# Kernel tuning notes

Measured on AMD Instinct MI355X. Metric: run time of the kernel, lower is better.

The kernel has to match this reference:

```python
import jax, jax.numpy as jnp
import numpy as np

B, L, D_MODEL, N_HEADS = 2, 1024, 1024, 8
KH = D_MODEL // 2 // N_HEADS   # key head dim = 64
VH = D_MODEL // N_HEADS        # value head dim = 128
SCALING = KH ** -0.5


def setup_inputs() -> dict:
    key = jax.random.key(0)
    ks = jax.random.split(key, 9)
    def w(k, shp):
        return jax.random.normal(k, shp, dtype=jnp.float32) / np.float32(np.sqrt(shp[0]))
    return {
        "x": jax.random.normal(ks[0], (B, L, D_MODEL), dtype=jnp.float32),
        "Wq": w(ks[1], (D_MODEL, D_MODEL // 2)),
        "Wk": w(ks[2], (D_MODEL, D_MODEL // 2)),
        "Wg1": w(ks[3], (D_MODEL, 16)),
        "Wg2": w(ks[4], (16, D_MODEL // 2)),
        "Wv": w(ks[5], (D_MODEL, D_MODEL)),
        "Wgp": w(ks[6], (D_MODEL, D_MODEL)),
        "bgp": jnp.zeros((D_MODEL,), jnp.float32),
        "Wout": w(ks[7], (D_MODEL, D_MODEL)),
    }


def _split_heads(t):
    # (b, l, h*d) -> (b, h, l, d)
    b, l, _ = t.shape
    return t.reshape(b, l, N_HEADS, -1).transpose(0, 2, 1, 3)


def _forward(x, Wq, Wk, Wg1, Wg2, Wv, Wgp, bgp, Wout):
    q = _split_heads(x @ Wq)                    # b h l kd
    k = _split_heads(x @ Wk) * SCALING          # b h l kd
    kg = _split_heads((x @ Wg1) @ Wg2)          # b h l kd (low-rank gate)
    v = _split_heads(x @ Wv)                    # b h l vd
    g = jax.nn.silu(x @ Wgp + bgp)              # b l d
    # per-head scalar decay gate in (0,1)
    gate = jnp.exp(jnp.mean(jax.nn.log_sigmoid(kg), axis=-1, keepdims=True) / 16.0)  # b h l 1
    prefix = jnp.cumprod(gate + 1e-6, axis=2)[..., None]                              # b h l 1 1
    kv = jnp.einsum('bhld,bhle->bhlde', k, v)                                         # b h l kd vd
    state = jnp.cumsum(kv / prefix, axis=2) * prefix                                  # decayed running KV state
    out = jnp.einsum('bhld,bhlde->bhle', q, state)                                    # b h l vd
    # LayerNorm over value head dim, no affine, eps=1e-5
    mu = out.mean(-1, keepdims=True)
    var = out.var(-1, keepdims=True)
    out = (out - mu) * jax.lax.rsqrt(var + 1e-5)
    out = out.transpose(0, 2, 1, 3).reshape(x.shape[0], x.shape[1], D_MODEL)
    return (g * out) @ Wout


def reference(x, Wq, Wk, Wg1, Wg2, Wv, Wgp, bgp, Wout):
    return _forward(x, Wq, Wk, Wg1, Wg2, Wv, Wgp, bgp, Wout)
```

## Files before the change

kernel.cpp:

```cpp
#include <hip/hip_runtime.h>

typedef __bf16 bf16x8 __attribute__((ext_vector_type(8)));
typedef float floatx4 __attribute__((ext_vector_type(4)));

__device__ __forceinline__ ushort f2bf(float f) {
  union { float f; unsigned u; } a; a.f = f;
  unsigned u = a.u;
  unsigned r = (u + 0x7FFFu + ((u >> 16) & 1u)) >> 16;
  return (ushort)r;
}
__device__ __forceinline__ float bf2f(ushort u) {
  union { unsigned u; float f; } a; a.u = ((unsigned)u) << 16;
  return a.f;
}

__device__ __forceinline__ void gl_lds16(const ushort* g, ushort* l) {
  __builtin_amdgcn_global_load_lds((const __attribute__((address_space(1))) void*)g,
                                   (__attribute__((address_space(3))) void*)l, 16, 0, 0);
}

#define SWZH(row, col, stride) ((((row) * (stride)) + (col)) ^ (((row) & 7) << 3))
#define SWZC(row, col) ((((row) * 128) + (col)) ^ ((((row) >> 3) & 7) << 2))


__global__ __launch_bounds__(256) void prep_all_kernel(
    const float* __restrict__ x,
    const float* __restrict__ Wq, const float* __restrict__ Wk,
    const float* __restrict__ Wv, const float* __restrict__ Wgp,
    const float* __restrict__ Wout,
    const float* __restrict__ Wg1, const float* __restrict__ Wg2,
    ushort* __restrict__ WcatT, ushort* __restrict__ WoutT,
    float* __restrict__ gamma, ushort* __restrict__ xb) {
  __shared__ __align__(16) float smem[1344];
  int bid = blockIdx.x;
  int tid = threadIdx.x;

  if (bid < 4096) {
    int nv = (bid & 127) * 32, k0 = (bid >> 7) * 32;
    const float* W; ushort* dst; int N, ncol, nrow; float scale = 1.f;
    if (nv < 512)       { W = Wq;   N = 512;  ncol = nv;         nrow = nv;        dst = WcatT; }
    else if (nv < 1024) { W = Wk;   N = 512;  ncol = nv - 512;   nrow = nv;        dst = WcatT; scale = 0.125f; }
    else if (nv < 2048) { W = Wv;   N = 1024; ncol = nv - 1024;  nrow = nv;        dst = WcatT; }
    else if (nv < 3072) { W = Wgp;  N = 1024; ncol = nv - 2048;  nrow = nv;        dst = WcatT; }
    else                { W = Wout; N = 1024; ncol = nv - 3072;  nrow = nv - 3072; dst = WoutT; }
    float* tile = smem;
    int xi = tid & 31, yi = tid >> 5;
    #pragma unroll
    for (int i = 0; i < 32; i += 8)
      tile[(yi + i) * 33 + xi] = W[(size_t)(k0 + yi + i) * N + ncol + xi];
    __syncthreads();
    #pragma unroll
    for (int i = 0; i < 32; i += 8)
      dst[(size_t)(nrow + yi + i) * 1024 + k0 + xi] = f2bf(tile[xi * 33 + yi + i] * scale);
    return;
  }

  int rowi = bid - 4096;
  int b = rowi >> 10, l = rowi & 1023;
  float* xrow = smem;
  float* part = smem + 1024;
  float* tsh  = smem + 1296;

  {
    float4 v = *(const float4*)(x + (size_t)rowi * 1024 + tid * 4);
    ushort4 o;
    o.x = f2bf(v.x); o.y = f2bf(v.y); o.z = f2bf(v.z); o.w = f2bf(v.w);
    *(ushort4*)(xb + (size_t)rowi * 1024 + tid * 4) = o;
    *(float4*)&xrow[tid * 4] = v;
  }
  __syncthreads();

  {
    int j = tid & 15, slice = tid >> 4;
    const float* xr = xrow + slice * 64;
    float p = 0.f;
    #pragma unroll 4
    for (int kk = 0; kk < 64; kk++)
      p += xr[kk] * Wg1[(size_t)(slice * 64 + kk) * 16 + j];
    part[slice * 17 + j] = p;
  }
  __syncthreads();
  if (tid < 16) {
    float s = 0.f;
    #pragma unroll
    for (int i = 0; i < 16; i++) s += part[i * 17 + tid];
    tsh[tid] = s;
  }
  __syncthreads();

  float ls0, ls1;
  {
    int n = tid;
    float kg = 0.f;
    #pragma unroll
    for (int j = 0; j < 16; j++) kg += tsh[j] * Wg2[j * 512 + n];
    ls0 = (kg >= 0.f) ? -log1pf(expf(-kg)) : (kg - log1pf(expf(kg)));
  }
  {
    int n = tid + 256;
    float kg = 0.f;
    #pragma unroll
    for (int j = 0; j < 16; j++) kg += tsh[j] * Wg2[j * 512 + n];
    ls1 = (kg >= 0.f) ? -log1pf(expf(-kg)) : (kg - log1pf(expf(kg)));
  }
  #pragma unroll
  for (int m = 32; m >= 1; m >>= 1) {
    ls0 += __shfl_xor(ls0, m);
    ls1 += __shfl_xor(ls1, m);
  }
  if ((tid & 63) == 0) {
    int w = tid >> 6;
    gamma[(size_t)(b * 8 + w) * 1024 + l]       = expf(ls0 * (1.f / 1024.f)) + 1e-6f;
    gamma[(size_t)(b * 8 + w + 4) * 1024 + l]   = expf(ls1 * (1.f / 1024.f)) + 1e-6f;
  }
}

__global__ __launch_bounds__(64) void prefix_kernel(const float* __restrict__ gamma,
                                                    float* __restrict__ af,
                                                    float* __restrict__ Atot) {
  int blk = blockIdx.x;
  int bh = blk >> 4, c = blk & 15;
  int lane = threadIdx.x;
  float g = gamma[(size_t)bh * 1024 + c * 64 + lane];
  #pragma unroll
  for (int m = 1; m < 64; m <<= 1) {
    float o = __shfl_up(g, m);
    if (lane >= m) g *= o;
  }
  af[(size_t)bh * 1024 + c * 64 + lane] = g;
  if (lane == 63) Atot[blk] = g;
}

__global__ __launch_bounds__(256) void gemm_proj_kernel(
    const ushort* __restrict__ A, const ushort* __restrict__ BT,
    const float* __restrict__ af, const float* __restrict__ Atot,
    const float* __restrict__ bgp,
    ushort* __restrict__ Qb, ushort* __restrict__ Kb,
    ushort* __restrict__ Ktb, ushort* __restrict__ Vtb,
    ushort* __restrict__ gsilu) {
  const int K = 1024;
  __shared__ __align__(16) char ldsraw[32768];
  ushort* As = (ushort*)ldsraw;
  ushort* Bs = (ushort*)(ldsraw + 8192);
  float*  Cs = (float*)ldsraw;
  __shared__ float ssh[2][64];
  __shared__ float bsh[128];

  int tid = threadIdx.x;
  int lane = tid & 63, wid = tid >> 6;
  int wr = wid >> 1, wc = wid & 1;
  int m0 = blockIdx.x * 64, n0 = blockIdx.y * 128;
  int by = blockIdx.y;
  int rtype = (by < 4) ? 0 : (by < 8) ? 1 : (by < 16) ? 2 : 3;
  int b = m0 >> 10, lbase = m0 & 1023, cch = lbase >> 6;

  if (rtype <= 1) {
    if (tid < 128) {
      int j = tid >> 6, li = tid & 63;
      int h = ((n0 - (rtype << 9)) >> 6) + j;
      int bh = b * 8 + h;
      float a = af[(size_t)bh * 1024 + lbase + li];
      ssh[j][li] = (rtype == 0) ? a : (Atot[bh * 16 + cch] / a);
    }
  } else if (rtype == 3) {
    if (tid < 128) bsh[tid] = bgp[n0 - 2048 + tid];
  }

  floatx4 acc[2][4];
  #pragma unroll
  for (int r = 0; r < 2; r++)
    #pragma unroll
    for (int c = 0; c < 4; c++)
      acc[r][c] = (floatx4){0.f, 0.f, 0.f, 0.f};

  int srA = wid * 16 + (lane >> 3);
  int srB = wid * 32 + (lane >> 3);
  int sc = (lane & 7) * 8;
  const ushort* ag = A + (size_t)(m0 + srA) * K + sc;
  const ushort* bg = BT + (size_t)(n0 + srB) * K + sc;
  ushort* asb = As + (wid * 16) * 64;
  ushort* bsb = Bs + (wid * 32) * 64;
  int row = lane & 15, kseg = (lane >> 4) << 3;

  for (int k0 = 0; k0 < K; k0 += 64) {
    __syncthreads();
    #pragma unroll
    for (int i = 0; i < 2; i++)
      gl_lds16(ag + (size_t)(i * 8) * K + k0, asb + i * 8 * 64);
    #pragma unroll
    for (int i = 0; i < 4; i++)
      gl_lds16(bg + (size_t)(i * 8) * K + k0, bsb + i * 8 * 64);
    __syncthreads();
    #pragma unroll
    for (int kk = 0; kk < 64; kk += 32) {
      bf16x8 av[2], bv[4];
      #pragma unroll
      for (int r = 0; r < 2; r++)
        av[r] = *(const bf16x8*)&As[(wr * 32 + r * 16 + row) * 64 + kk + kseg];
      #pragma unroll
      for (int c = 0; c < 4; c++)
        bv[c] = *(const bf16x8*)&Bs[(wc * 64 + c * 16 + row) * 64 + kk + kseg];
      #pragma unroll
      for (int r = 0; r < 2; r++)
        #pragma unroll
        for (int c = 0; c < 4; c++)
          acc[r][c] = __builtin_amdgcn_mfma_f32_16x16x32_bf16(av[r], bv[c], acc[r][c], 0, 0, 0);
    }
  }

  __syncthreads();
  #pragma unroll
  for (int r = 0; r < 2; r++) {
    int crow = wr * 32 + r * 16 + ((lane >> 4) << 2);
    #pragma unroll
    for (int c = 0; c < 4; c++) {
      int ccol = wc * 64 + c * 16 + (lane & 15);
      #pragma unroll
      for (int i = 0; i < 4; i++)
        Cs[SWZC(crow + i, ccol)] = acc[r][c][i];
    }
  }
  __syncthreads();

  if (rtype == 0) {
    #pragma unroll
    for (int it = 0; it < 4; it++) {
      int u = tid + it * 256;
      int rw = u >> 4, col8 = (u & 15) * 8;
      int hh = col8 >> 6, d = col8 & 63;
      float a = ssh[hh][rw];
      float4 v0 = *(const float4*)&Cs[SWZC(rw, col8)];
      float4 v1 = *(const float4*)&Cs[SWZC(rw, col8 + 4)];
      ushort o[8];
      o[0]=f2bf(v0.x*a); o[1]=f2bf(v0.y*a); o[2]=f2bf(v0.z*a); o[3]=f2bf(v0.w*a);
      o[4]=f2bf(v1.x*a); o[5]=f2bf(v1.y*a); o[6]=f2bf(v1.z*a); o[7]=f2bf(v1.w*a);
      int bh = b * 8 + (n0 >> 6) + hh;
      *(uint4*)(Qb + ((size_t)bh * 1024 + lbase + rw) * 64 + d) = *(uint4*)&o[0];
    }
  } else if (rtype == 1) {
    #pragma unroll
    for (int it = 0; it < 4; it++) {
      int u = tid + it * 256;
      int rw = u >> 4, col8 = (u & 15) * 8;
      int hh = col8 >> 6, d = col8 & 63;
      float4 v0 = *(const float4*)&Cs[SWZC(rw, col8)];
      float4 v1 = *(const float4*)&Cs[SWZC(rw, col8 + 4)];
      ushort o[8];
      o[0]=f2bf(v0.x); o[1]=f2bf(v0.y); o[2]=f2bf(v0.z); o[3]=f2bf(v0.w);
      o[4]=f2bf(v1.x); o[5]=f2bf(v1.y); o[6]=f2bf(v1.z); o[7]=f2bf(v1.w);
      int bh = b * 8 + ((n0 - 512) >> 6) + hh;
      *(uint4*)(Kb + ((size_t)bh * 1024 + lbase + rw) * 64 + d) = *(uint4*)&o[0];
    }
    #pragma unroll
    for (int it = 0; it < 4; it++) {
      int u = tid + it * 256;
      int l0 = (u & 7) * 8, dd = (u >> 3) & 63, hh = u >> 9;
      ushort o[8];
      #pragma unroll
      for (int j = 0; j < 8; j++)
        o[j] = f2bf(Cs[SWZC(l0 + j, hh * 64 + dd)] * ssh[hh][l0 + j]);
      int bh = b * 8 + ((n0 - 512) >> 6) + hh;
      *(uint4*)(Ktb + ((size_t)(bh * 64 + dd)) * 1024 + lbase + l0) = *(uint4*)&o[0];
    }
  } else if (rtype == 2) {
    #pragma unroll
    for (int it = 0; it < 4; it++) {
      int u = tid + it * 256;
      int l0 = (u & 7) * 8, e = u >> 3;
      ushort o[8];
      #pragma unroll
      for (int j = 0; j < 8; j++)
        o[j] = f2bf(Cs[SWZC(l0 + j, e)]);
      int bh = b * 8 + ((n0 - 1024) >> 7);
      *(uint4*)(Vtb + ((size_t)(bh * 128 + e)) * 1024 + lbase + l0) = *(uint4*)&o[0];
    }
  } else {
    #pragma unroll
    for (int it = 0; it < 4; it++) {
      int u = tid + it * 256;
      int rw = u >> 4, col8 = (u & 15) * 8;
      float4 v0 = *(const float4*)&Cs[SWZC(rw, col8)];
      float4 v1 = *(const float4*)&Cs[SWZC(rw, col8 + 4)];
      float vv[8] = {v0.x, v0.y, v0.z, v0.w, v1.x, v1.y, v1.z, v1.w};
      ushort o[8];
      #pragma unroll
      for (int j = 0; j < 8; j++) {
        float z = vv[j] + bsh[col8 + j];
        o[j] = f2bf(z / (1.f + expf(-z)));
      }
      *(uint4*)(gsilu + (size_t)(m0 + rw) * 1024 + (n0 - 2048) + col8) = *(uint4*)&o[0];
    }
  }
}

__global__ __launch_bounds__(256) void chunk_T_kernel(const ushort* __restrict__ Ktb,
                                                      const ushort* __restrict__ Vtb,
                                                      float* __restrict__ Tt) {
  int c = blockIdx.x, bh = blockIdx.y;
  int tid = threadIdx.x;
  int lane = tid & 63, wid = tid >> 6;
  int col_l = lane & 15, kseg8 = (lane >> 4) * 8;
  int d0w = wid * 16;

  __shared__ __align__(16) ushort Kt[64 * 64];
  __shared__ __align__(16) ushort Vs[128 * 64];

  #pragma unroll
  for (int i = 0; i < 2; i++) {
    int u = tid + i * 256;
    int row = u >> 3, col8 = u & 7;
    *(uint4*)&Kt[SWZH(row, col8 * 8, 64)] =
        *(const uint4*)(Ktb + ((size_t)(bh * 64 + row)) * 1024 + c * 64 + col8 * 8);
  }
  #pragma unroll
  for (int i = 0; i < 4; i++) {
    int u = tid + i * 256;
    int row = u >> 3, col8 = u & 7;
    *(uint4*)&Vs[SWZH(row, col8 * 8, 64)] =
        *(const uint4*)(Vtb + ((size_t)(bh * 128 + row)) * 1024 + c * 64 + col8 * 8);
  }
  __syncthreads();

  floatx4 acc[8];
  #pragma unroll
  for (int i = 0; i < 8; i++) acc[i] = (floatx4){0.f, 0.f, 0.f, 0.f};

  #pragma unroll
  for (int kk = 0; kk < 64; kk += 32) {
    bf16x8 kb = *(const bf16x8*)&Kt[SWZH(d0w + col_l, kk + kseg8, 64)];
    #pragma unroll
    for (int fe = 0; fe < 8; fe++) {
      bf16x8 vb = *(const bf16x8*)&Vs[SWZH(fe * 16 + col_l, kk + kseg8, 64)];
      acc[fe] = __builtin_amdgcn_mfma_f32_16x16x32_bf16(vb, kb, acc[fe], 0, 0, 0);
    }
  }

  float* To = Tt + (size_t)(bh * 16 + c) * 8192;
  #pragma unroll
  for (int fe = 0; fe < 8; fe++) {
    #pragma unroll
    for (int r = 0; r < 4; r++) {
      int e = fe * 16 + (lane >> 4) * 4 + r;
      To[(size_t)e * 64 + d0w + col_l] = acc[fe][r];
    }
  }
}

__global__ __launch_bounds__(256) void state_kernel(const float* __restrict__ Tt,
                                                    const float* __restrict__ Atot,
                                                    ushort* __restrict__ Stb) {
  int es = blockIdx.x, bh = blockIdx.y;
  int tid = threadIdx.x;
  size_t off = (size_t)es * 512 + tid * 2;
  float2 S = {0.f, 0.f};
  for (int c = 0; c < 16; c++) {
    float A = Atot[bh * 16 + c];
    size_t base = (size_t)(bh * 16 + c) * 8192 + off;
    ushort2 o; o.x = f2bf(S.x); o.y = f2bf(S.y);
    *(ushort2*)(Stb + base) = o;
    float2 t = *(const float2*)(Tt + base);
    S.x = A * S.x + t.x;
    S.y = A * S.y + t.y;
  }
}

__global__ __launch_bounds__(256) void out_chunk_kernel(const float* __restrict__ af,
                                                        const ushort* __restrict__ Qb,
                                                        const ushort* __restrict__ Kb,
                                                        const ushort* __restrict__ Stb,
                                                        const ushort* __restrict__ Vtb,
                                                        const ushort* __restrict__ gsilu,
                                                        ushort* __restrict__ gout) {
  int c = blockIdx.x, bh = blockIdx.y;
  int b = bh >> 3, h = bh & 7;
  int tid = threadIdx.x;
  int lane = tid & 63, wid = tid >> 6;
  int col_l = lane & 15, kseg8 = (lane >> 4) * 8;
  int t0w = wid * 16;

  __shared__ __align__(16) ushort Qs[64 * 64];
  __shared__ __align__(16) ushort Ks[64 * 64];
  __shared__ __align__(16) ushort Ss[128 * 64];
  __shared__ __align__(16) ushort Vs[128 * 64];
  __shared__ __align__(16) ushort Ps[64 * 64];
  __shared__ __align__(16) ushort Gz[64 * 128];
  __shared__ float inva_sh[64];

  #pragma unroll
  for (int i = 0; i < 2; i++) {
    int u = tid + i * 256;
    int row = u >> 3, col8 = u & 7;
    *(uint4*)&Qs[SWZH(row, col8 * 8, 64)] =
        *(const uint4*)(Qb + ((size_t)(bh * 1024 + c * 64 + row)) * 64 + col8 * 8);
    *(uint4*)&Ks[SWZH(row, col8 * 8, 64)] =
        *(const uint4*)(Kb + ((size_t)(bh * 1024 + c * 64 + row)) * 64 + col8 * 8);
  }
  #pragma unroll
  for (int i = 0; i < 4; i++) {
    int u = tid + i * 256;
    int row = u >> 3, col8 = u & 7;
    *(uint4*)&Ss[SWZH(row, col8 * 8, 64)] =
        *(const uint4*)(Stb + (size_t)(bh * 16 + c) * 8192 + (size_t)row * 64 + col8 * 8);
    *(uint4*)&Vs[SWZH(row, col8 * 8, 64)] =
        *(const uint4*)(Vtb + ((size_t)(bh * 128 + row)) * 1024 + c * 64 + col8 * 8);
  }
  #pragma unroll
  for (int i = 0; i < 4; i++) {
    int u = tid + i * 256;
    int row = u >> 4, ch = u & 15;
    *(uint4*)&Gz[SWZH(row, ch * 8, 128)] =
        *(const uint4*)(gsilu + ((size_t)(b * 1024 + c * 64 + row)) * 1024 + h * 128 + ch * 8);
  }
  if (tid < 64) inva_sh[tid] = 1.f / af[(size_t)bh * 1024 + c * 64 + tid];
  __syncthreads();

  floatx4 pacc[4];
  floatx4 acc[8];
  #pragma unroll
  for (int i = 0; i < 4; i++) pacc[i] = (floatx4){0.f, 0.f, 0.f, 0.f};
  #pragma unroll
  for (int i = 0; i < 8; i++) acc[i] = (floatx4){0.f, 0.f, 0.f, 0.f};

  #pragma unroll
  for (int kk = 0; kk < 64; kk += 32) {
    bf16x8 qb = *(const bf16x8*)&Qs[SWZH(t0w + col_l, kk + kseg8, 64)];
    #pragma unroll
    for (int fs = 0; fs < 4; fs++) {
      bf16x8 kb = *(const bf16x8*)&Ks[SWZH(fs * 16 + col_l, kk + kseg8, 64)];
      pacc[fs] = __builtin_amdgcn_mfma_f32_16x16x32_bf16(kb, qb, pacc[fs], 0, 0, 0);
    }
    #pragma unroll
    for (int fe = 0; fe < 8; fe++) {
      bf16x8 sb = *(const bf16x8*)&Ss[SWZH(fe * 16 + col_l, kk + kseg8, 64)];
      acc[fe] = __builtin_amdgcn_mfma_f32_16x16x32_bf16(sb, qb, acc[fe], 0, 0, 0);
    }
  }

  int tl = t0w + col_l;
  #pragma unroll
  for (int fs = 0; fs < 4; fs++) {
    ushort o[4];
    #pragma unroll
    for (int r = 0; r < 4; r++) {
      int s = fs * 16 + (lane >> 4) * 4 + r;
      float pv = (s <= tl) ? pacc[fs][r] * inva_sh[s] : 0.f;
      o[r] = f2bf(pv);
    }
    int s0 = fs * 16 + (lane >> 4) * 4;
    *(ushort4*)&Ps[SWZH(tl, s0, 64)] = *(ushort4*)&o[0];
  }
  __syncthreads();

  #pragma unroll
  for (int kk = 0; kk < 64; kk += 32) {
    bf16x8 pb = *(const bf16x8*)&Ps[SWZH(t0w + col_l, kk + kseg8, 64)];
    #pragma unroll
    for (int fe = 0; fe < 8; fe++) {
      bf16x8 vb = *(const bf16x8*)&Vs[SWZH(fe * 16 + col_l, kk + kseg8, 64)];
      acc[fe] = __builtin_amdgcn_mfma_f32_16x16x32_bf16(vb, pb, acc[fe], 0, 0, 0);
    }
  }
  __syncthreads();

  float s1 = 0.f, s2 = 0.f;
  #pragma unroll
  for (int fe = 0; fe < 8; fe++)
    #pragma unroll
    for (int r = 0; r < 4; r++) {
      float v = acc[fe][r];
      s1 += v; s2 += v * v;
    }
  s1 += __shfl_xor(s1, 16); s2 += __shfl_xor(s2, 16);
  s1 += __shfl_xor(s1, 32); s2 += __shfl_xor(s2, 32);
  float mu = s1 * (1.f / 128.f);
  float var = s2 * (1.f / 128.f) - mu * mu;
  float rs = rsqrtf(var + 1e-5f);

  ushort* Gs = Vs;
  #pragma unroll
  for (int fe = 0; fe < 8; fe++)
    #pragma unroll
    for (int r = 0; r < 4; r++) {
      int e = fe * 16 + (lane >> 4) * 4 + r;
      float y = (acc[fe][r] - mu) * rs;
      float g = bf2f(Gz[SWZH(tl, e, 128)]);
      Gs[SWZH(tl, e, 128)] = f2bf(y * g);
    }
  __syncthreads();

  #pragma unroll
  for (int i = 0; i < 4; i++) {
    int u = tid + i * 256;
    int row = u >> 4, ch = u & 15;
    *(uint4*)(gout + ((size_t)(b * 1024 + c * 64 + row)) * 1024 + h * 128 + ch * 8) =
        *(uint4*)&Gs[SWZH(row, ch * 8, 128)];
  }
}

__global__ __launch_bounds__(256) void gemm_out_kernel(const ushort* __restrict__ A,
                                                       const ushort* __restrict__ BT,
                                                       float* __restrict__ C) {
  const int K = 1024, N = 1024;
  __shared__ __align__(16) ushort As[64 * 64];
  __shared__ __align__(16) ushort Bs[128 * 64];
  int tid = threadIdx.x;
  int lane = tid & 63, wid = tid >> 6;
  int wr = wid >> 1, wc = wid & 1;
  int m0 = blockIdx.x * 64, n0 = blockIdx.y * 128;
  int row = lane & 15, kseg = (lane >> 4) << 3;

  floatx4 acc[2][4];
  #pragma unroll
  for (int r = 0; r < 2; r++)
    #pragma unroll
    for (int c = 0; c < 4; c++)
      acc[r][c] = (floatx4){0.f, 0.f, 0.f, 0.f};

  int srowA = wid * 16 + (lane >> 3);
  int srowB = wid * 32 + (lane >> 3);
  int scol = (lane & 7) * 8;
  const ushort* ag = A + (size_t)(m0 + srowA) * K + scol;
  const ushort* bg = BT + (size_t)(n0 + srowB) * K + scol;
  ushort* asb = As + (wid * 16) * 64;
  ushort* bsb = Bs + (wid * 32) * 64;

  for (int k0 = 0; k0 < K; k0 += 64) {
    __syncthreads();
    #pragma unroll
    for (int i = 0; i < 2; i++)
      gl_lds16(ag + (size_t)(i * 8) * K + k0, asb + i * 8 * 64);
    #pragma unroll
    for (int i = 0; i < 4; i++)
      gl_lds16(bg + (size_t)(i * 8) * K + k0, bsb + i * 8 * 64);
    __syncthreads();
    #pragma unroll
    for (int kk = 0; kk < 64; kk += 32) {
      bf16x8 av[2], bv[4];
      #pragma unroll
      for (int r = 0; r < 2; r++)
        av[r] = *(const bf16x8*)&As[(wr * 32 + r * 16 + row) * 64 + kk + kseg];
      #pragma unroll
      for (int c = 0; c < 4; c++)
        bv[c] = *(const bf16x8*)&Bs[(wc * 64 + c * 16 + row) * 64 + kk + kseg];
      #pragma unroll
      for (int r = 0; r < 2; r++)
        #pragma unroll
        for (int c = 0; c < 4; c++)
          acc[r][c] = __builtin_amdgcn_mfma_f32_16x16x32_bf16(av[r], bv[c], acc[r][c], 0, 0, 0);
    }
  }

  int r4 = (lane >> 4) << 2;
  #pragma unroll
  for (int r = 0; r < 2; r++)
    #pragma unroll
    for (int c = 0; c < 4; c++) {
      int crow = m0 + wr * 32 + r * 16 + r4;
      int ccol = n0 + wc * 64 + c * 16 + (lane & 15);
      #pragma unroll
      for (int i = 0; i < 4; i++)
        C[(size_t)(crow + i) * N + ccol] = acc[r][c][i];
    }
}

extern "C" void kernel_launch(void* const* d_in, const int* in_sizes, int n_in,
                              void* d_out, int out_size, void* d_ws, size_t ws_size,
                              hipStream_t stream) {
  const float* x    = (const float*)d_in[0];
  const float* Wq   = (const float*)d_in[1];
  const float* Wk   = (const float*)d_in[2];
  const float* Wg1  = (const float*)d_in[3];
  const float* Wg2  = (const float*)d_in[4];
  const float* Wv   = (const float*)d_in[5];
  const float* Wgp  = (const float*)d_in[6];
  const float* bgp  = (const float*)d_in[7];
  const float* Wout = (const float*)d_in[8];
  float* out = (float*)d_out;

  char* ws = (char*)d_ws;
  float*  Tt     = (float*)(ws + 0);
  ushort* Stb    = (ushort*)(ws + 8388608);
  float*  gamma  = (float*)(ws + 12582912);
  float*  af     = (float*)(ws + 12648448);
  float*  Atot   = (float*)(ws + 12713984);
  ushort* Qb     = (ushort*)(ws + 12718080);
  ushort* Kb     = (ushort*)(ws + 14815232);
  ushort* Ktb    = (ushort*)(ws + 16912384);
  ushort* Vtb    = (ushort*)(ws + 19009536);
  ushort* xb     = (ushort*)(ws + 23203840);
  ushort* WcatT  = (ushort*)(ws + 27398144);
  ushort* WoutT  = (ushort*)(ws + 33689600);
  ushort* gout   = (ushort*)(ws + 35786752);
  ushort* gsilu  = (ushort*)(ws + 39981056);

  prep_all_kernel<<<6144, 256, 0, stream>>>(x, Wq, Wk, Wv, Wgp, Wout, Wg1, Wg2,
                                            WcatT, WoutT, gamma, xb);
  prefix_kernel<<<256, 64, 0, stream>>>(gamma, af, Atot);

  gemm_proj_kernel<<<dim3(32, 24), 256, 0, stream>>>(xb, WcatT, af, Atot, bgp,
                                                     Qb, Kb, Ktb, Vtb, gsilu);

  chunk_T_kernel<<<dim3(16, 16), 256, 0, stream>>>(Ktb, Vtb, Tt);
  state_kernel<<<dim3(16, 16), 256, 0, stream>>>(Tt, Atot, Stb);
  out_chunk_kernel<<<dim3(16, 16), 256, 0, stream>>>(af, Qb, Kb, Stb, Vtb, gsilu, gout);

  gemm_out_kernel<<<dim3(32, 8), 256, 0, stream>>>(gout, WoutT, out);
}
```

Baseline: 87.41 us.

## Fuse prefix scan into consumer kernels and double threads in chunk kernels

```diff
diff --git a/kernel.cpp b/kernel.cpp
--- a/kernel.cpp
+++ b/kernel.cpp
@@ -17,6 +17,16 @@
 __device__ __forceinline__ void gl_lds16(const ushort* g, ushort* l) {
   __builtin_amdgcn_global_load_lds((const __attribute__((address_space(1))) void*)g,
                                    (__attribute__((address_space(3))) void*)l, 16, 0, 0);
+}
+
+__device__ __forceinline__ float chunk_scan(float g) {
+  int lane = threadIdx.x & 63;
+  #pragma unroll
+  for (int m = 1; m < 64; m <<= 1) {
+    float o = __shfl_up(g, m);
+    if (lane >= m) g *= o;
+  }
+  return g;
 }
 
 #define SWZH(row, col, stride) ((((row) * (stride)) + (col)) ^ (((row) & 7) << 3))
@@ -115,26 +125,9 @@
   }
 }
 
-__global__ __launch_bounds__(64) void prefix_kernel(const float* __restrict__ gamma,
-                                                    float* __restrict__ af,
-                                                    float* __restrict__ Atot) {
-  int blk = blockIdx.x;
-  int bh = blk >> 4, c = blk & 15;
-  int lane = threadIdx.x;
-  float g = gamma[(size_t)bh * 1024 + c * 64 + lane];
-  #pragma unroll
-  for (int m = 1; m < 64; m <<= 1) {
-    float o = __shfl_up(g, m);
-    if (lane >= m) g *= o;
-  }
-  af[(size_t)bh * 1024 + c * 64 + lane] = g;
-  if (lane == 63) Atot[blk] = g;
-}
-
 __global__ __launch_bounds__(256) void gemm_proj_kernel(
     const ushort* __restrict__ A, const ushort* __restrict__ BT,
-    const float* __restrict__ af, const float* __restrict__ Atot,
-    const float* __restrict__ bgp,
+    const float* __restrict__ gamma, const float* __restrict__ bgp,
     ushort* __restrict__ Qb, ushort* __restrict__ Kb,
     ushort* __restrict__ Ktb, ushort* __restrict__ Vtb,
     ushort* __restrict__ gsilu) {
@@ -152,16 +145,14 @@
   int m0 = blockIdx.x * 64, n0 = blockIdx.y * 128;
   int by = blockIdx.y;
   int rtype = (by < 4) ? 0 : (by < 8) ? 1 : (by < 16) ? 2 : 3;
-  int b = m0 >> 10, lbase = m0 & 1023, cch = lbase >> 6;
-
-  if (rtype <= 1) {
-    if (tid < 128) {
-      int j = tid >> 6, li = tid & 63;
-      int h = ((n0 - (rtype << 9)) >> 6) + j;
-      int bh = b * 8 + h;
-      float a = af[(size_t)bh * 1024 + lbase + li];
-      ssh[j][li] = (rtype == 0) ? a : (Atot[bh * 16 + cch] / a);
-    }
+  int b = m0 >> 10, lbase = m0 & 1023;
+
+  if (rtype <= 1 && wid < 2) {
+    int h = ((n0 - (rtype << 9)) >> 6) + wid;
+    int bh = b * 8 + h;
+    float a = chunk_scan(gamma[(size_t)bh * 1024 + lbase + lane]);
+    float Ac = __shfl(a, 63);
+    ssh[wid][lane] = (rtype == 0) ? a : (Ac / a);
   } else if (rtype == 3) {
     if (tid < 128) bsh[tid] = bgp[n0 - 2048 + tid];
   }
@@ -293,68 +284,78 @@
   }
 }
 
-__global__ __launch_bounds__(256) void chunk_T_kernel(const ushort* __restrict__ Ktb,
+__global__ __launch_bounds__(512) void chunk_T_kernel(const ushort* __restrict__ Ktb,
                                                       const ushort* __restrict__ Vtb,
                                                       float* __restrict__ Tt) {
   int c = blockIdx.x, bh = blockIdx.y;
   int tid = threadIdx.x;
   int lane = tid & 63, wid = tid >> 6;
+  int wq = wid & 3, eh = wid >> 2;
   int col_l = lane & 15, kseg8 = (lane >> 4) * 8;
-  int d0w = wid * 16;
+  int d0w = wq * 16;
 
   __shared__ __align__(16) ushort Kt[64 * 64];
   __shared__ __align__(16) ushort Vs[128 * 64];
 
-  #pragma unroll
-  for (int i = 0; i < 2; i++) {
-    int u = tid + i * 256;
-    int row = u >> 3, col8 = u & 7;
+  {
+    int row = tid >> 3, col8 = tid & 7;
     *(uint4*)&Kt[SWZH(row, col8 * 8, 64)] =
         *(const uint4*)(Ktb + ((size_t)(bh * 64 + row)) * 1024 + c * 64 + col8 * 8);
   }
   #pragma unroll
-  for (int i = 0; i < 4; i++) {
-    int u = tid + i * 256;
+  for (int i = 0; i < 2; i++) {
+    int u = tid + i * 512;
     int row = u >> 3, col8 = u & 7;
     *(uint4*)&Vs[SWZH(row, col8 * 8, 64)] =
         *(const uint4*)(Vtb + ((size_t)(bh * 128 + row)) * 1024 + c * 64 + col8 * 8);
   }
   __syncthreads();
 
-  floatx4 acc[8];
-  #pragma unroll
-  for (int i = 0; i < 8; i++) acc[i] = (floatx4){0.f, 0.f, 0.f, 0.f};
+  floatx4 acc[4];
+  #pragma unroll
+  for (int i = 0; i < 4; i++) acc[i] = (floatx4){0.f, 0.f, 0.f, 0.f};
 
   #pragma unroll
   for (int kk = 0; kk < 64; kk += 32) {
     bf16x8 kb = *(const bf16x8*)&Kt[SWZH(d0w + col_l, kk + kseg8, 64)];
     #pragma unroll
-    for (int fe = 0; fe < 8; fe++) {
-      bf16x8 vb = *(const bf16x8*)&Vs[SWZH(fe * 16 + col_l, kk + kseg8, 64)];
-      acc[fe] = __builtin_amdgcn_mfma_f32_16x16x32_bf16(vb, kb, acc[fe], 0, 0, 0);
+    for (int j = 0; j < 4; j++) {
+      bf16x8 vb = *(const bf16x8*)&Vs[SWZH((eh * 4 + j) * 16 + col_l, kk + kseg8, 64)];
+      acc[j] = __builtin_amdgcn_mfma_f32_16x16x32_bf16(vb, kb, acc[j], 0, 0, 0);
     }
   }
 
   float* To = Tt + (size_t)(bh * 16 + c) * 8192;
   #pragma unroll
-  for (int fe = 0; fe < 8; fe++) {
+  for (int j = 0; j < 4; j++) {
     #pragma unroll
     for (int r = 0; r < 4; r++) {
-      int e = fe * 16 + (lane >> 4) * 4 + r;
-      To[(size_t)e * 64 + d0w + col_l] = acc[fe][r];
+      int e = (eh * 4 + j) * 16 + (lane >> 4) * 4 + r;
+      To[(size_t)e * 64 + d0w + col_l] = acc[j][r];
     }
   }
 }
 
 __global__ __launch_bounds__(256) void state_kernel(const float* __restrict__ Tt,
-                                                    const float* __restrict__ Atot,
+                                                    const float* __restrict__ gamma,
                                                     ushort* __restrict__ Stb) {
   int es = blockIdx.x, bh = blockIdx.y;
   int tid = threadIdx.x;
+  int lane = tid & 63, wid = tid >> 6;
+  __shared__ float Atot_sh[16];
+
+  #pragma unroll
+  for (int j = 0; j < 4; j++) {
+    int cc = wid * 4 + j;
+    float a = chunk_scan(gamma[(size_t)bh * 1024 + cc * 64 + lane]);
+    if (lane == 63) Atot_sh[cc] = a;
+  }
+  __syncthreads();
+
   size_t off = (size_t)es * 512 + tid * 2;
   float2 S = {0.f, 0.f};
   for (int c = 0; c < 16; c++) {
-    float A = Atot[bh * 16 + c];
+    float A = Atot_sh[c];
     size_t base = (size_t)(bh * 16 + c) * 8192 + off;
     ushort2 o; o.x = f2bf(S.x); o.y = f2bf(S.y);
     *(ushort2*)(Stb + base) = o;
@@ -364,7 +365,7 @@
   }
 }
 
-__global__ __launch_bounds__(256) void out_chunk_kernel(const float* __restrict__ af,
+__global__ __launch_bounds__(512) void out_chunk_kernel(const float* __restrict__ gamma,
                                                         const ushort* __restrict__ Qb,
                                                         const ushort* __restrict__ Kb,
                                                         const ushort* __restrict__ Stb,
@@ -375,8 +376,9 @@
   int b = bh >> 3, h = bh & 7;
   int tid = threadIdx.x;
   int lane = tid & 63, wid = tid >> 6;
+  int wq = wid & 3, eh = wid >> 2;
   int col_l = lane & 15, kseg8 = (lane >> 4) * 8;
-  int t0w = wid * 16;
+  int t0w = wq * 16;
 
   __shared__ __align__(16) ushort Qs[64 * 64];
   __shared__ __align__(16) ushort Ks[64 * 64];
@@ -385,19 +387,23 @@
   __shared__ __align__(16) ushort Ps[64 * 64];
   __shared__ __align__(16) ushort Gz[64 * 128];
   __shared__ float inva_sh[64];
-
-  #pragma unroll
-  for (int i = 0; i < 2; i++) {
-    int u = tid + i * 256;
-    int row = u >> 3, col8 = u & 7;
+  __shared__ float2 red[2][4][16];
+
+  if (wid == 0) {
+    float a = chunk_scan(gamma[(size_t)bh * 1024 + c * 64 + lane]);
+    inva_sh[lane] = 1.f / a;
+  }
+
+  {
+    int row = tid >> 3, col8 = tid & 7;
     *(uint4*)&Qs[SWZH(row, col8 * 8, 64)] =
         *(const uint4*)(Qb + ((size_t)(bh * 1024 + c * 64 + row)) * 64 + col8 * 8);
     *(uint4*)&Ks[SWZH(row, col8 * 8, 64)] =
         *(const uint4*)(Kb + ((size_t)(bh * 1024 + c * 64 + row)) * 64 + col8 * 8);
   }
   #pragma unroll
-  for (int i = 0; i < 4; i++) {
-    int u = tid + i * 256;
+  for (int i = 0; i < 2; i++) {
+    int u = tid + i * 512;
     int row = u >> 3, col8 = u & 7;
     *(uint4*)&Ss[SWZH(row, col8 * 8, 64)] =
         *(const uint4*)(Stb + (size_t)(bh * 16 + c) * 8192 + (size_t)row * 64 + col8 * 8);
@@ -405,45 +411,47 @@
         *(const uint4*)(Vtb + ((size_t)(bh * 128 + row)) * 1024 + c * 64 + col8 * 8);
   }
   #pragma unroll
-  for (int i = 0; i < 4; i++) {
-    int u = tid + i * 256;
+  for (int i = 0; i < 2; i++) {
+    int u = tid + i * 512;
     int row = u >> 4, ch = u & 15;
     *(uint4*)&Gz[SWZH(row, ch * 8, 128)] =
         *(const uint4*)(gsilu + ((size_t)(b * 1024 + c * 64 + row)) * 1024 + h * 128 + ch * 8);
   }
-  if (tid < 64) inva_sh[tid] = 1.f / af[(size_t)bh * 1024 + c * 64 + tid];
-  __syncthreads();
-
-  floatx4 pacc[4];
-  floatx4 acc[8];
-  #pragma unroll
-  for (int i = 0; i < 4; i++) pacc[i] = (floatx4){0.f, 0.f, 0.f, 0.f};
-  #pragma unroll
-  for (int i = 0; i < 8; i++) acc[i] = (floatx4){0.f, 0.f, 0.f, 0.f};
+  __syncthreads();
+
+  floatx4 pacc[2];
+  floatx4 acc[4];
+  #pragma unroll
+  for (int i = 0; i < 2; i++) pacc[i] = (floatx4){0.f, 0.f, 0.f, 0.f};
+  #pragma unroll
+  for (int i = 0; i < 4; i++) acc[i] = (floatx4){0.f, 0.f, 0.f, 0.f};
 
   #pragma unroll
   for (int kk = 0; kk < 64; kk += 32) {
     bf16x8 qb = *(const bf16x8*)&Qs[SWZH(t0w + col_l, kk + kseg8, 64)];
     #pragma unroll
-    for (int fs = 0; fs < 4; fs++) {
+    for (int j = 0; j < 2; j++) {
+      int fs = eh * 2 + j;
       bf16x8 kb = *(const bf16x8*)&Ks[SWZH(fs * 16 + col_l, kk + kseg8, 64)];
-      pacc[fs] = __builtin_amdgcn_mfma_f32_16x16x32_bf16(kb, qb, pacc[fs], 0, 0, 0);
-    }
-    #pragma unroll
-    for (int fe = 0; fe < 8; fe++) {
+      pacc[j] = __builtin_amdgcn_mfma_f32_16x16x32_bf16(kb, qb, pacc[j], 0, 0, 0);
+    }
+    #pragma unroll
+    for (int j = 0; j < 4; j++) {
+      int fe = eh * 4 + j;
       bf16x8 sb = *(const bf16x8*)&Ss[SWZH(fe * 16 + col_l, kk + kseg8, 64)];
-      acc[fe] = __builtin_amdgcn_mfma_f32_16x16x32_bf16(sb, qb, acc[fe], 0, 0, 0);
+      acc[j] = __builtin_amdgcn_mfma_f32_16x16x32_bf16(sb, qb, acc[j], 0, 0, 0);
     }
   }
 
   int tl = t0w + col_l;
   #pragma unroll
-  for (int fs = 0; fs < 4; fs++) {
+  for (int j = 0; j < 2; j++) {
+    int fs = eh * 2 + j;
     ushort o[4];
     #pragma unroll
     for (int r = 0; r < 4; r++) {
       int s = fs * 16 + (lane >> 4) * 4 + r;
-      float pv = (s <= tl) ? pacc[fs][r] * inva_sh[s] : 0.f;
+      float pv = (s <= tl) ? pacc[j][r] * inva_sh[s] : 0.f;
       o[r] = f2bf(pv);
     }
     int s0 = fs * 16 + (lane >> 4) * 4;
@@ -455,42 +463,47 @@
   for (int kk = 0; kk < 64; kk += 32) {
     bf16x8 pb = *(const bf16x8*)&Ps[SWZH(t0w + col_l, kk + kseg8, 64)];
     #pragma unroll
-    for (int fe = 0; fe < 8; fe++) {
+    for (int j = 0; j < 4; j++) {
+      int fe = eh * 4 + j;
       bf16x8 vb = *(const bf16x8*)&Vs[SWZH(fe * 16 + col_l, kk + kseg8, 64)];
-      acc[fe] = __builtin_amdgcn_mfma_f32_16x16x32_bf16(vb, pb, acc[fe], 0, 0, 0);
+      acc[j] = __builtin_amdgcn_mfma_f32_16x16x32_bf16(vb, pb, acc[j], 0, 0, 0);
     }
   }
   __syncthreads();
 
   float s1 = 0.f, s2 = 0.f;
   #pragma unroll
-  for (int fe = 0; fe < 8; fe++)
+  for (int j = 0; j < 4; j++)
     #pragma unroll
     for (int r = 0; r < 4; r++) {
-      float v = acc[fe][r];
+      float v = acc[j][r];
       s1 += v; s2 += v * v;
     }
   s1 += __shfl_xor(s1, 16); s2 += __shfl_xor(s2, 16);
   s1 += __shfl_xor(s1, 32); s2 += __shfl_xor(s2, 32);
-  float mu = s1 * (1.f / 128.f);
-  float var = s2 * (1.f / 128.f) - mu * mu;
+  if (lane < 16) red[eh][wq][lane] = make_float2(s1, s2);
+  __syncthreads();
+  float2 oth = red[1 - eh][wq][col_l];
+  float S1 = s1 + oth.x, S2 = s2 + oth.y;
+  float mu = S1 * (1.f / 128.f);
+  float var = S2 * (1.f / 128.f) - mu * mu;
   float rs = rsqrtf(var + 1e-5f);
 
   ushort* Gs = Vs;
   #pragma unroll
-  for (int fe = 0; fe < 8; fe++)
+  for (int j = 0; j < 4; j++)
     #pragma unroll
     for (int r = 0; r < 4; r++) {
-      int e = fe * 16 + (lane >> 4) * 4 + r;
-      float y = (acc[fe][r] - mu) * rs;
+      int e = (eh * 4 + j) * 16 + (lane >> 4) * 4 + r;
+      float y = (acc[j][r] - mu) * rs;
       float g = bf2f(Gz[SWZH(tl, e, 128)]);
       Gs[SWZH(tl, e, 128)] = f2bf(y * g);
     }
   __syncthreads();
 
   #pragma unroll
-  for (int i = 0; i < 4; i++) {
-    int u = tid + i * 256;
+  for (int i = 0; i < 2; i++) {
+    int u = tid + i * 512;
     int row = u >> 4, ch = u & 15;
     *(uint4*)(gout + ((size_t)(b * 1024 + c * 64 + row)) * 1024 + h * 128 + ch * 8) =
         *(uint4*)&Gs[SWZH(row, ch * 8, 128)];
@@ -581,8 +594,6 @@
   float*  Tt     = (float*)(ws + 0);
   ushort* Stb    = (ushort*)(ws + 8388608);
   float*  gamma  = (float*)(ws + 12582912);
-  float*  af     = (float*)(ws + 12648448);
-  float*  Atot   = (float*)(ws + 12713984);
   ushort* Qb     = (ushort*)(ws + 12718080);
   ushort* Kb     = (ushort*)(ws + 14815232);
   ushort* Ktb    = (ushort*)(ws + 16912384);
@@ -595,14 +606,13 @@
 
   prep_all_kernel<<<6144, 256, 0, stream>>>(x, Wq, Wk, Wv, Wgp, Wout, Wg1, Wg2,
                                             WcatT, WoutT, gamma, xb);
-  prefix_kernel<<<256, 64, 0, stream>>>(gamma, af, Atot);
-
-  gemm_proj_kernel<<<dim3(32, 24), 256, 0, stream>>>(xb, WcatT, af, Atot, bgp,
+
+  gemm_proj_kernel<<<dim3(32, 24), 256, 0, stream>>>(xb, WcatT, gamma, bgp,
                                                      Qb, Kb, Ktb, Vtb, gsilu);
 
-  chunk_T_kernel<<<dim3(16, 16), 256, 0, stream>>>(Ktb, Vtb, Tt);
-  state_kernel<<<dim3(16, 16), 256, 0, stream>>>(Tt, Atot, Stb);
-  out_chunk_kernel<<<dim3(16, 16), 256, 0, stream>>>(af, Qb, Kb, Stb, Vtb, gsilu, gout);
+  chunk_T_kernel<<<dim3(16, 16), 512, 0, stream>>>(Ktb, Vtb, Tt);
+  state_kernel<<<dim3(16, 16), 256, 0, stream>>>(Tt, gamma, Stb);
+  out_chunk_kernel<<<dim3(16, 16), 512, 0, stream>>>(gamma, Qb, Kb, Stb, Vtb, gsilu, gout);
 
   gemm_out_kernel<<<dim3(32, 8), 256, 0, stream>>>(gout, WoutT, out);
 }
```

Result: no change. 85.91 us (-1.7%).
